# Optimization experiments

Measured on AMD Instinct MI355X. Metric: run time of the kernel, lower is better.

Reference implementation:

```python
import jax, jax.numpy as jnp
import numpy as np
from jax import lax

DN = ('NHWC', 'HWIO', 'NHWC')
OUTPUT_STRIDE = 2
PEAK_THRESHOLD = 0.2


def setup_inputs() -> dict:
    key = jax.random.key(0)
    k1, k2, k3 = jax.random.split(key, 3)
    crops = jax.random.normal(k1, (128, 192, 192, 1), dtype=jnp.float32)
    # simple confmap backbone: stride-2 conv -> relu -> 3x3 conv to 17 nodes
    W1 = jax.random.normal(k2, (3, 3, 1, 32), dtype=jnp.float32) * 0.1
    b1 = jnp.zeros((32,), dtype=jnp.float32)
    W2 = jax.random.normal(k3, (3, 3, 32, 17), dtype=jnp.float32) * 0.1
    b2 = jnp.zeros((17,), dtype=jnp.float32)
    return {"crops": crops, "W1": W1, "b1": b1, "W2": W2, "b2": b2}


def _confmaps(crops, W1, b1, W2, b2):
    # keras_model forward: (B, 192, 192, 1) -> (B, 96, 96, 17), output_stride = 2
    h = lax.conv_general_dilated(crops, W1, (2, 2), 'SAME', dimension_numbers=DN) + b1
    h = jax.nn.relu(h)
    cms = lax.conv_general_dilated(h, W2, (1, 1), 'SAME', dimension_numbers=DN) + b2
    return cms


def _find_global_peaks_local(cms, threshold):
    # cms: (B, H, W, N) -> peaks (B, N, 2) in (x, y), vals (B, N)
    B, H, W, N = cms.shape
    cm = jnp.transpose(cms, (0, 3, 1, 2)).reshape(B, N, H * W)  # (B, N, HW)
    flat_idx = jnp.argmax(cm, axis=-1)                           # (B, N)
    vals = jnp.take_along_axis(cm, flat_idx[..., None], axis=-1)[..., 0]
    yi = flat_idx // W
    xi = flat_idx % W

    def gather(yy, xx):
        yy = jnp.clip(yy, 0, H - 1)
        xx = jnp.clip(xx, 0, W - 1)
        return jnp.take_along_axis(cm, (yy * W + xx)[..., None], axis=-1)[..., 0]

    # quarter-pixel local gradient offset (refinement='local')
    dx = 0.25 * jnp.sign(gather(yi, xi + 1) - gather(yi, xi - 1))
    dy = 0.25 * jnp.sign(gather(yi + 1, xi) - gather(yi - 1, xi))

    pts = jnp.stack([xi.astype(cm.dtype) + dx, yi.astype(cm.dtype) + dy], axis=-1)
    pts = jnp.where(vals[..., None] >= threshold, pts, jnp.nan)
    return pts, vals


def reference(crops, W1, b1, W2, b2):
    # preprocess: inputs already float grayscale, input_scale=1.0 -> identity
    cms = _confmaps(crops, W1, b1, W2, b2)
    peak_points, peak_vals = _find_global_peaks_local(cms, PEAK_THRESHOLD)
    peak_points = peak_points * OUTPUT_STRIDE  # adjust to input image grid
    # pack (x, y, val) into one array: (B, nodes, 3)
    return jnp.concatenate([peak_points, peak_vals[..., None]], axis=-1)
```

## Files before the change

kernel.cpp:

```cpp
#include <hip/hip_runtime.h>


#define NCH 17
#define C1 32
#define TW 24
#define TH 32
#define HT_W 26
#define HT_H 34
#define HSTR 28
#define IN_W 53
#define IN_H 69
#define CG 8
#define NG 4
#define NHPX (HT_H * HT_W)
#define SH_PLANE (HT_H * HSTR)

__device__ __forceinline__ unsigned long long pack_key(float v, unsigned flat) {
    unsigned ub = __float_as_uint(v);
    ub = (ub & 0x80000000u) ? ~ub : (ub | 0x80000000u);
    return ((unsigned long long)ub << 32) | (unsigned)(~flat);
}

__global__ __launch_bounds__(256, 3) void conv_peaks_kernel(
    const float* __restrict__ crops, const float* __restrict__ W1g,
    const float* __restrict__ b1g, const float* __restrict__ W2g,
    const float* __restrict__ b2g, unsigned long long* __restrict__ peaks) {
    __shared__ __align__(16) float s_in[IN_H * IN_W];
    __shared__ __align__(16) float s_h[CG * SH_PLANE];

    const int t = threadIdx.x;
    const int b = blockIdx.y;
    const int ty0 = (blockIdx.x >> 2) * TH;
    const int tx0 = (blockIdx.x & 3) * TW;
    const int iy0 = 2 * ty0 - 2;
    const int ix0 = 2 * tx0 - 2;
    const float* cb = crops + b * 192 * 192;

    for (int p = t; p < IN_H * IN_W; p += 256) {
        int r = p / IN_W, cc = p - r * IN_W;
        int iy = iy0 + r, ix = ix0 + cc;
        float v = 0.f;
        if (iy >= 0 && ix >= 0 && iy < 192 && ix < 192) v = cb[iy * 192 + ix];
        s_in[p] = v;
    }

    const int ly = t >> 3;
    const int lx0 = (t & 7) * 3;
    float acc[NCH][3];
#pragma unroll
    for (int n = 0; n < NCH; ++n)
#pragma unroll
        for (int p = 0; p < 3; ++p) acc[n][p] = 0.f;

#pragma unroll 1
    for (int g = 0; g < NG; ++g) {
        __syncthreads();

#pragma unroll
        for (int i = 0; i < 4; ++i) {
            int p = t + i * 256;
            if (i < 3 || t < NHPX - 768) {
                int r = p / HT_W, cc = p - r * HT_W;
                int hy = ty0 - 1 + r, hx = tx0 - 1 + cc;
                float vf = (hy >= 0 && hy < 96 && hx >= 0 && hx < 96) ? 1.f : 0.f;
                const float* ip = s_in + 2 * r * IN_W + 2 * cc;
                float in9[9];
#pragma unroll
                for (int qy = 0; qy < 3; ++qy)
#pragma unroll
                    for (int qx = 0; qx < 3; ++qx)
                        in9[qy * 3 + qx] = ip[qy * IN_W + qx];
#pragma unroll
                for (int cl = 0; cl < CG; ++cl) {
                    const int c = g * CG + cl;
                    float a = b1g[c];
#pragma unroll
                    for (int q = 0; q < 9; ++q)
                        a = fmaf(in9[q], W1g[q * C1 + c], a);
                    s_h[cl * SH_PLANE + r * HSTR + cc] = fmaxf(a, 0.f) * vf;
                }
            }
        }
        __syncthreads();

#pragma unroll 1
        for (int cl = 0; cl < CG; ++cl) {
            const float* hp = s_h + cl * SH_PLANE + ly * HSTR + lx0;
            float hr[3][5];
#pragma unroll
            for (int ky = 0; ky < 3; ++ky)
#pragma unroll
                for (int j = 0; j < 5; ++j) hr[ky][j] = hp[ky * HSTR + j];
            const int c = g * CG + cl;
#pragma unroll
            for (int k = 0; k < 9; ++k) {
                const int ky = k / 3, kx = k - ky * 3;
                const float* wb = W2g + (k * C1 + c) * NCH;
                float w[NCH];
#pragma unroll
                for (int n = 0; n < NCH; ++n) w[n] = wb[n];
#pragma unroll
                for (int p = 0; p < 3; ++p) {
                    const float h = hr[ky][kx + p];
#pragma unroll
                    for (int n = 0; n < NCH; ++n)
                        acc[n][p] = fmaf(h, w[n], acc[n][p]);
                }
            }
        }
    }

    const int yg = ty0 + ly, xg = tx0 + lx0;
    const int lane = t & 63;
#pragma unroll
    for (int n = 0; n < NCH; ++n) {
        const float bb = b2g[n];
        unsigned long long pk = pack_key(acc[n][0] + bb, (unsigned)(yg * 96 + xg));
#pragma unroll
        for (int p = 1; p < 3; ++p) {
            unsigned long long o = pack_key(acc[n][p] + bb, (unsigned)(yg * 96 + xg + p));
            if (o > pk) pk = o;
        }
#pragma unroll
        for (int off = 32; off; off >>= 1) {
            unsigned long long o = __shfl_down(pk, off, 64);
            if (o > pk) pk = o;
        }
        if (lane == 0) atomicMax(&peaks[b * NCH + n], pk);
    }
}

__global__ __launch_bounds__(64) void refine_kernel(
    const float* __restrict__ crops, const float* __restrict__ W1g,
    const float* __restrict__ b1g, const float* __restrict__ W2g,
    const unsigned long long* __restrict__ peaks, float* __restrict__ out) {
    const int bn = blockIdx.x;
    const int b = bn / NCH, n = bn % NCH;
    const int lane = threadIdx.x;

    unsigned long long pk = peaks[bn];
    unsigned key = (unsigned)(pk >> 32);
    unsigned fbits = (key & 0x80000000u) ? (key ^ 0x80000000u) : ~key;
    float val = __uint_as_float(fbits);
    int flat = (int)(~(unsigned)(pk & 0xffffffffu));
    int yi = flat / 96, xi = flat - yi * 96;

    const int j = lane >> 4;
    int yy = yi + ((j == 2) ? 1 : 0) - ((j == 3) ? 1 : 0);
    int xx = xi + ((j == 0) ? 1 : 0) - ((j == 1) ? 1 : 0);
    yy = min(max(yy, 0), 95);
    xx = min(max(xx, 0), 95);

    const float* cb = crops + b * 192 * 192;
    float pat[7][7];
#pragma unroll
    for (int r = 0; r < 7; ++r) {
        int iy = 2 * yy - 2 + r;
#pragma unroll
        for (int s = 0; s < 7; ++s) {
            int ix = 2 * xx - 2 + s;
            pat[r][s] = (iy >= 0 && iy < 192 && ix >= 0 && ix < 192)
                            ? cb[iy * 192 + ix] : 0.f;
        }
    }

    float part = 0.f;
#pragma unroll
    for (int ci = 0; ci < 2; ++ci) {
        const int c = (lane & 15) + ci * 16;
        const float bias = b1g[c];
        float w1[9];
#pragma unroll
        for (int q = 0; q < 9; ++q) w1[q] = W1g[q * C1 + c];
#pragma unroll
        for (int dy = 0; dy < 3; ++dy) {
#pragma unroll
            for (int dx = 0; dx < 3; ++dx) {
                int hy = yy - 1 + dy, hx = xx - 1 + dx;
                if (hy >= 0 && hy < 96 && hx >= 0 && hx < 96) {
                    float a = bias;
#pragma unroll
                    for (int qy = 0; qy < 3; ++qy)
#pragma unroll
                        for (int qx = 0; qx < 3; ++qx)
                            a = fmaf(pat[2 * dy + qy][2 * dx + qx],
                                     w1[qy * 3 + qx], a);
                    float hval = fmaxf(a, 0.f);
                    part = fmaf(hval, W2g[((dy * 3 + dx) * C1 + c) * NCH + n], part);
                }
            }
        }
    }
    for (int off = 8; off; off >>= 1) part += __shfl_down(part, off, 16);
    float g0 = __shfl(part, 0, 64);
    float g1 = __shfl(part, 16, 64);
    float g2 = __shfl(part, 32, 64);
    float g3 = __shfl(part, 48, 64);

    if (lane == 0) {
        float d0 = g0 - g1, d1 = g2 - g3;
        float sx = (d0 > 0.f) ? 1.f : ((d0 < 0.f) ? -1.f : 0.f);
        float sy = (d1 > 0.f) ? 1.f : ((d1 < 0.f) ? -1.f : 0.f);
        float px = ((float)xi + 0.25f * sx) * 2.f;
        float py = ((float)yi + 0.25f * sy) * 2.f;
        if (!(val >= 0.2f)) {
            px = __int_as_float(0x7fc00000);
            py = __int_as_float(0x7fc00000);
        }
        out[bn * 3 + 0] = px;
        out[bn * 3 + 1] = py;
        out[bn * 3 + 2] = val;
    }
}

extern "C" void kernel_launch(void* const* d_in, const int* in_sizes, int n_in,
                              void* d_out, int out_size, void* d_ws, size_t ws_size,
                              hipStream_t stream) {
    const float* crops = (const float*)d_in[0];
    const float* W1 = (const float*)d_in[1];
    const float* b1 = (const float*)d_in[2];
    const float* W2 = (const float*)d_in[3];
    const float* b2 = (const float*)d_in[4];
    float* out = (float*)d_out;
    unsigned long long* peaks = (unsigned long long*)d_ws;

    hipMemsetAsync(d_ws, 0, 128 * NCH * sizeof(unsigned long long), stream);

    dim3 gridB(12, 128);
    conv_peaks_kernel<<<gridB, 256, 0, stream>>>(crops, W1, b1, W2, b2, peaks);
    refine_kernel<<<128 * NCH, 64, 0, stream>>>(crops, W1, b1, W2, peaks, out);
}
```

Measured before the change: 227.2 us.

## Apply Winograd F(2,3) along x for the second convolution

Replaces the direct 3x3 conv2 inner loop with a 1-D Winograd F(2,3) transform along the x axis. Each thread now computes 4 outputs, two Winograd pairs, using 4 transformed weights per ky instead of 3 taps per output, which cuts multiplies per output. A small setup kernel pretransforms W2 into workspace each call. The block shrinks to 192 threads with occupancy hint 2, the h-tile offsets are hoisted, and the LDS stride is padded to 29. The trade-off is more accumulator registers (17x2x4) and an extra kernel launch, plus slightly different float rounding in the argmax that could flip ties.

```diff
diff --git a/kernel.cpp b/kernel.cpp
--- a/kernel.cpp
+++ b/kernel.cpp
@@ -7,13 +7,15 @@
 #define TH 32
 #define HT_W 26
 #define HT_H 34
-#define HSTR 28
+#define HSTR 29
 #define IN_W 53
 #define IN_H 69
 #define CG 8
 #define NG 4
+#define NT 192
 #define NHPX (HT_H * HT_W)
 #define SH_PLANE (HT_H * HSTR)
+#define WT_OFF 17408
 
 __device__ __forceinline__ unsigned long long pack_key(float v, unsigned flat) {
     unsigned ub = __float_as_uint(v);
@@ -21,9 +23,25 @@
     return ((unsigned long long)ub << 32) | (unsigned)(~flat);
 }
 
-__global__ __launch_bounds__(256, 3) void conv_peaks_kernel(
+__global__ void wt_setup_kernel(const float* __restrict__ W2g,
+                                float* __restrict__ Wt) {
+    int i = blockIdx.x * 256 + threadIdx.x;
+    if (i >= 3 * C1 * NCH) return;
+    int n = i % NCH, rem = i / NCH;
+    int c = rem % C1, ky = rem / C1;
+    float g0 = W2g[((ky * 3 + 0) * C1 + c) * NCH + n];
+    float g1 = W2g[((ky * 3 + 1) * C1 + c) * NCH + n];
+    float g2 = W2g[((ky * 3 + 2) * C1 + c) * NCH + n];
+    float* o = Wt + ((ky * C1 + c) * 4) * NCH + n;
+    o[0 * NCH] = g0;
+    o[1 * NCH] = 0.5f * (g0 + g1 + g2);
+    o[2 * NCH] = 0.5f * (g0 - g1 + g2);
+    o[3 * NCH] = g2;
+}
+
+__global__ __launch_bounds__(NT, 2) void conv_peaks_kernel(
     const float* __restrict__ crops, const float* __restrict__ W1g,
-    const float* __restrict__ b1g, const float* __restrict__ W2g,
+    const float* __restrict__ b1g, const float* __restrict__ Wtg,
     const float* __restrict__ b2g, unsigned long long* __restrict__ peaks) {
     __shared__ __align__(16) float s_in[IN_H * IN_W];
     __shared__ __align__(16) float s_h[CG * SH_PLANE];
@@ -36,7 +54,7 @@
     const int ix0 = 2 * tx0 - 2;
     const float* cb = crops + b * 192 * 192;
 
-    for (int p = t; p < IN_H * IN_W; p += 256) {
+    for (int p = t; p < IN_H * IN_W; p += NT) {
         int r = p / IN_W, cc = p - r * IN_W;
         int iy = iy0 + r, ix = ix0 + cc;
         float v = 0.f;
@@ -44,26 +62,36 @@
         s_in[p] = v;
     }
 
-    const int ly = t >> 3;
-    const int lx0 = (t & 7) * 3;
-    float acc[NCH][3];
+    int in_off[5], out_off[5];
+    float vf[5];
+#pragma unroll
+    for (int i = 0; i < 5; ++i) {
+        int p = t + i * NT;
+        int r = p / HT_W, cc = p - r * HT_W;
+        int hy = ty0 - 1 + r, hx = tx0 - 1 + cc;
+        vf[i] = (hy >= 0 && hy < 96 && hx >= 0 && hx < 96) ? 1.f : 0.f;
+        in_off[i] = 2 * r * IN_W + 2 * cc;
+        out_off[i] = r * HSTR + cc;
+    }
+
+    const int ly = t / 6;
+    const int lx0 = (t - ly * 6) * 4;
+    float macc[NCH][2][4];
 #pragma unroll
     for (int n = 0; n < NCH; ++n)
 #pragma unroll
-        for (int p = 0; p < 3; ++p) acc[n][p] = 0.f;
+        for (int pr = 0; pr < 2; ++pr)
+#pragma unroll
+            for (int j = 0; j < 4; ++j) macc[n][pr][j] = 0.f;
 
 #pragma unroll 1
     for (int g = 0; g < NG; ++g) {
         __syncthreads();
 
 #pragma unroll
-        for (int i = 0; i < 4; ++i) {
-            int p = t + i * 256;
-            if (i < 3 || t < NHPX - 768) {
-                int r = p / HT_W, cc = p - r * HT_W;
-                int hy = ty0 - 1 + r, hx = tx0 - 1 + cc;
-                float vf = (hy >= 0 && hy < 96 && hx >= 0 && hx < 96) ? 1.f : 0.f;
-                const float* ip = s_in + 2 * r * IN_W + 2 * cc;
+        for (int i = 0; i < 5; ++i) {
+            if (i < 4 || t < NHPX - 4 * NT) {
+                const float* ip = s_in + in_off[i];
                 float in9[9];
 #pragma unroll
                 for (int qy = 0; qy < 3; ++qy)
@@ -77,7 +105,7 @@
 #pragma unroll
                     for (int q = 0; q < 9; ++q)
                         a = fmaf(in9[q], W1g[q * C1 + c], a);
-                    s_h[cl * SH_PLANE + r * HSTR + cc] = fmaxf(a, 0.f) * vf;
+                    s_h[cl * SH_PLANE + out_off[i]] = fmaxf(a, 0.f) * vf[i];
                 }
             }
         }
@@ -85,27 +113,27 @@
 
 #pragma unroll 1
         for (int cl = 0; cl < CG; ++cl) {
+            const int c = g * CG + cl;
             const float* hp = s_h + cl * SH_PLANE + ly * HSTR + lx0;
-            float hr[3][5];
-#pragma unroll
-            for (int ky = 0; ky < 3; ++ky)
-#pragma unroll
-                for (int j = 0; j < 5; ++j) hr[ky][j] = hp[ky * HSTR + j];
-            const int c = g * CG + cl;
-#pragma unroll
-            for (int k = 0; k < 9; ++k) {
-                const int ky = k / 3, kx = k - ky * 3;
-                const float* wb = W2g + (k * C1 + c) * NCH;
-                float w[NCH];
-#pragma unroll
-                for (int n = 0; n < NCH; ++n) w[n] = wb[n];
-#pragma unroll
-                for (int p = 0; p < 3; ++p) {
-                    const float h = hr[ky][kx + p];
-#pragma unroll
-                    for (int n = 0; n < NCH; ++n)
-                        acc[n][p] = fmaf(h, w[n], acc[n][p]);
-                }
+#pragma unroll
+            for (int ky = 0; ky < 3; ++ky) {
+                float d[6];
+#pragma unroll
+                for (int j = 0; j < 6; ++j) d[j] = hp[ky * HSTR + j];
+                float pa[4], pb[4];
+                pa[0] = d[0] - d[2]; pa[1] = d[1] + d[2];
+                pa[2] = d[2] - d[1]; pa[3] = d[1] - d[3];
+                pb[0] = d[2] - d[4]; pb[1] = d[3] + d[4];
+                pb[2] = d[4] - d[3]; pb[3] = d[3] - d[5];
+                const float* wb = Wtg + ((ky * C1 + c) * 4) * NCH;
+#pragma unroll
+                for (int j = 0; j < 4; ++j)
+#pragma unroll
+                    for (int n = 0; n < NCH; ++n) {
+                        const float wv = wb[j * NCH + n];
+                        macc[n][0][j] = fmaf(pa[j], wv, macc[n][0][j]);
+                        macc[n][1][j] = fmaf(pb[j], wv, macc[n][1][j]);
+                    }
             }
         }
     }
@@ -115,12 +143,15 @@
 #pragma unroll
     for (int n = 0; n < NCH; ++n) {
         const float bb = b2g[n];
-        unsigned long long pk = pack_key(acc[n][0] + bb, (unsigned)(yg * 96 + xg));
-#pragma unroll
-        for (int p = 1; p < 3; ++p) {
-            unsigned long long o = pack_key(acc[n][p] + bb, (unsigned)(yg * 96 + xg + p));
-            if (o > pk) pk = o;
-        }
+        float o0 = macc[n][0][0] + macc[n][0][1] + macc[n][0][2] + bb;
+        float o1 = macc[n][0][1] - macc[n][0][2] - macc[n][0][3] + bb;
+        float o2 = macc[n][1][0] + macc[n][1][1] + macc[n][1][2] + bb;
+        float o3 = macc[n][1][1] - macc[n][1][2] - macc[n][1][3] + bb;
+        float mv = o0; int am = 0;
+        if (o1 > mv) { mv = o1; am = 1; }
+        if (o2 > mv) { mv = o2; am = 2; }
+        if (o3 > mv) { mv = o3; am = 3; }
+        unsigned long long pk = pack_key(mv, (unsigned)(yg * 96 + xg + am));
 #pragma unroll
         for (int off = 32; off; off >>= 1) {
             unsigned long long o = __shfl_down(pk, off, 64);
@@ -223,10 +254,12 @@
     const float* b2 = (const float*)d_in[4];
     float* out = (float*)d_out;
     unsigned long long* peaks = (unsigned long long*)d_ws;
+    float* Wt = (float*)((char*)d_ws + WT_OFF);
 
     hipMemsetAsync(d_ws, 0, 128 * NCH * sizeof(unsigned long long), stream);
+    wt_setup_kernel<<<7, 256, 0, stream>>>(W2, Wt);
 
     dim3 gridB(12, 128);
-    conv_peaks_kernel<<<gridB, 256, 0, stream>>>(crops, W1, b1, W2, b2, peaks);
+    conv_peaks_kernel<<<gridB, NT, 0, stream>>>(crops, W1, b1, Wt, b2, peaks);
     refine_kernel<<<128 * NCH, 64, 0, stream>>>(crops, W1, b1, W2, peaks, out);
 }
```

Measured after the change: 681.8 us. 3x slower.
